# Kernel optimization log

Hardware: AMD Instinct MI355X
Metric: run time of the kernel (lower is better)

Reference implementation:

```python
import jax, jax.numpy as jnp
import numpy as np


def segment_softmax(x, seg, num_segments):
    # numerically-stable softmax over graph segments (rows of the sparse matrix)
    m = jax.ops.segment_max(x, seg, num_segments=num_segments)
    e = jnp.exp(x - m[seg])
    s = jax.ops.segment_sum(e, seg, num_segments=num_segments)
    return e / s[seg]


def setup_inputs() -> dict:
    key = jax.random.key(0)
    ks = jax.random.split(key, 12)
    B, N, E, P, H = 256, 51200, 102400, 5, 300
    instruction = jax.random.normal(ks[0], (B, H), dtype=jnp.float32)
    distribution = jax.random.uniform(ks[1], (N,), dtype=jnp.float32)
    node_attrs = jax.random.normal(ks[2], (N, H), dtype=jnp.float32)
    edge_attrs = jax.random.normal(ks[3], (E, H), dtype=jnp.float32)
    node_indices = jnp.sort(jax.random.randint(ks[4], (N,), 0, B)).astype(jnp.int32)
    edge_batch_indices = jax.random.randint(ks[5], (E,), 0, B).astype(jnp.int32)
    edge_indices = jax.random.randint(ks[6], (2, E), 0, N).astype(jnp.int32)
    prop_embeds = jax.random.normal(ks[7], (P, H), dtype=jnp.float32)
    Ws_property = jax.random.uniform(ks[8], (P, H, H), dtype=jnp.float32)
    W_state = jax.random.uniform(ks[9], (H,), dtype=jnp.float32)
    W_relation = jax.random.uniform(ks[10], (H,), dtype=jnp.float32)
    return {"instruction": instruction, "distribution": distribution, "node_attrs": node_attrs,
            "edge_attrs": edge_attrs, "node_indices": node_indices,
            "edge_batch_indices": edge_batch_indices, "edge_indices": edge_indices,
            "prop_embeds": prop_embeds, "Ws_property": Ws_property,
            "W_state": W_state, "W_relation": W_relation}


def reference(instruction, distribution, node_attrs, edge_attrs, node_indices,
              edge_batch_indices, edge_indices, prop_embeds, Ws_property,
              W_state, W_relation):
    B = instruction.shape[0]
    # [B, P] property similarities
    prop_sim = jax.nn.softmax(instruction @ prop_embeds.T, axis=1)
    ps_node = prop_sim[node_indices]            # [N, P]
    instr_node = instruction[node_indices]      # [N, H]
    # per-property transform of node attrs: [N, P-1, H]
    wx = jnp.einsum('phk,nk->nph', Ws_property[:-1], node_attrs)
    node_scores = jax.nn.elu(jnp.sum(ps_node[:, :-1, None] * instr_node[:, None, :] * wx, axis=1))  # [N, H]
    # relation transform of edge attrs: [E, H]
    edge_wx = jnp.einsum('hk,ek->eh', Ws_property[-1], edge_attrs)
    edge_scores = jax.nn.elu(instruction[edge_batch_indices] * edge_wx)  # [E, H]
    # per-graph (segment) softmax over state logits
    state_logits = node_scores @ W_state        # [N]
    next_states = segment_softmax(state_logits, node_indices, B)
    # scatter-add message passing: dst node accumulates distribution[src] * edge_scores
    agg = jnp.zeros_like(node_scores).at[edge_indices[1]].add(
        distribution[edge_indices[0], None] * edge_scores)  # [N, H]
    rel_logits = agg @ W_relation               # [N]
    next_relations = segment_softmax(rel_logits, node_indices, B)
    r = ps_node[:, -1]
    next_distribution = r * next_relations + (1.0 - r) * next_states
    return next_distribution, prop_sim
```

## Files before the change

kernel.cpp:

```cpp
#include <hip/hip_runtime.h>
#include <math.h>

#define H 300
#define PP 5
#define NE 128
#define KC 32
#define NCH 10
#define ROWB 128
#define WTILE (320 * ROWB)
#define WHALF (160 * ROWB)
#define ATILE (NE * ROWB)
#define NTHREADS 256
#define GT 512

using short8 = __attribute__((ext_vector_type(8))) short;
using f32x4  = __attribute__((ext_vector_type(4))) float;

__device__ __forceinline__ float wsum64(float v) {
#pragma unroll
    for (int m = 32; m >= 1; m >>= 1) v += __shfl_xor(v, m, 64);
    return v;
}
__device__ __forceinline__ float wmax64(float v) {
#pragma unroll
    for (int m = 32; m >= 1; m >>= 1) v = fmaxf(v, __shfl_xor(v, m, 64));
    return v;
}
__device__ __forceinline__ float eluf(float x) { return x > 0.f ? x : expm1f(x); }

__device__ __forceinline__ unsigned short f2bf(float x) {
    unsigned int u = __float_as_uint(x);
    unsigned int r = u + 0x7FFF + ((u >> 16) & 1);
    return (unsigned short)(r >> 16);
}
__device__ __forceinline__ float bf2f(unsigned short h) {
    return __uint_as_float(((unsigned int)h) << 16);
}
__device__ __forceinline__ int sw(int r, int kb) {
    return r * ROWB + (kb ^ ((r & 7) << 4));
}
__device__ __forceinline__ void split4(const float* v, uint2& ph, uint2& pl) {
    unsigned short hs[4], ls[4];
#pragma unroll
    for (int i = 0; i < 4; ++i) {
        hs[i] = f2bf(v[i]);
        ls[i] = f2bf(v[i] - bf2f(hs[i]));
    }
    ph = make_uint2((unsigned)hs[0] | ((unsigned)hs[1] << 16),
                    (unsigned)hs[2] | ((unsigned)hs[3] << 16));
    pl = make_uint2((unsigned)ls[0] | ((unsigned)ls[1] << 16),
                    (unsigned)ls[2] | ((unsigned)ls[3] << 16));
}
__device__ __forceinline__ void gload16(const void* g, void* lds) {
    __builtin_amdgcn_global_load_lds(
        (const __attribute__((address_space(1))) unsigned int*)g,
        (__attribute__((address_space(3))) unsigned int*)lds, 16, 0, 0);
}
#define SBAR() __builtin_amdgcn_s_barrier()
#define SCHED() __builtin_amdgcn_sched_barrier(0)
#define WAIT_LGKM() asm volatile("s_waitcnt lgkmcnt(0)" ::: "memory")
#define WAIT_VM0()  asm volatile("s_waitcnt vmcnt(0)" ::: "memory")
#define WAIT_VM4()  asm volatile("s_waitcnt vmcnt(4)" ::: "memory")
#define WAIT_VM5()  asm volatile("s_waitcnt vmcnt(5)" ::: "memory")

__global__ void k_prop_sim(const float* __restrict__ instr,
                           const float* __restrict__ pe,
                           float* __restrict__ prop_sim) {
    int b = blockIdx.x, lane = threadIdx.x;
    float dots[PP];
#pragma unroll
    for (int p = 0; p < PP; ++p) {
        float s = 0.f;
        for (int hh = lane; hh < H; hh += 64) s += instr[b * H + hh] * pe[p * H + hh];
        dots[p] = wsum64(s);
    }
    if (lane == 0) {
        float m = dots[0];
#pragma unroll
        for (int p = 1; p < PP; ++p) m = fmaxf(m, dots[p]);
        float e[PP], s = 0.f;
#pragma unroll
        for (int p = 0; p < PP; ++p) { e[p] = expf(dots[p] - m); s += e[p]; }
        float inv = 1.f / s;
#pragma unroll
        for (int p = 0; p < PP; ++p) prop_sim[b * PP + p] = e[p] * inv;
    }
}

__global__ void k_counts(const int* __restrict__ idx, int* __restrict__ counts, int N) {
    int i = blockIdx.x * blockDim.x + threadIdx.x;
    if (i < N) atomicAdd(&counts[idx[i]], 1);
}

__global__ void k_scan(const int* __restrict__ counts, int* __restrict__ offsets, int B) {
    __shared__ int sh[256];
    int t = threadIdx.x;
    int c = (t < B) ? counts[t] : 0;
    sh[t] = c;
    __syncthreads();
    for (int off = 1; off < 256; off <<= 1) {
        int v = (t >= off) ? sh[t - off] : 0;
        __syncthreads();
        sh[t] += v;
        __syncthreads();
    }
    if (t < B) offsets[t] = sh[t] - c;
    if (t == B - 1) offsets[B] = sh[t];
}

__global__ void k_presplit(const float* __restrict__ W4, char* __restrict__ img) {
    int c = blockIdx.x;
    int idx = blockIdx.y * NTHREADS + threadIdx.x;
    int r = idx >> 3, j = idx & 7;
    int k = c * KC + j * 4;
    float v[4] = {0.f, 0.f, 0.f, 0.f};
    if (r < H && k < H) *(float4*)v = *(const float4*)&W4[(size_t)r * H + k];
    uint2 ph, pl;
    split4(v, ph, pl);
    char* row = img + (size_t)c * WTILE + (size_t)r * ROWB;
    int x = (r & 7) << 4;
    *(uint2*)(row + ((j * 8) ^ x)) = ph;
    *(uint2*)(row + ((64 + j * 8) ^ x)) = pl;
}

__global__ void k_combine(const float* __restrict__ Ws,
                          const float* __restrict__ prop_sim,
                          const float* __restrict__ instr,
                          char* __restrict__ img) {
    int b = blockIdx.x, c = blockIdx.y, t = threadIdx.x;
    float ps0 = prop_sim[b * PP + 0], ps1 = prop_sim[b * PP + 1];
    float ps2 = prop_sim[b * PP + 2], ps3 = prop_sim[b * PP + 3];
    char* tile = img + ((size_t)b * NCH + c) * WTILE;
#pragma unroll
    for (int i = 0; i < 10; ++i) {
        int idx = t + i * NTHREADS;
        int r = idx >> 3, j = idx & 7;
        int k = c * KC + j * 4;
        float cv[4] = {0.f, 0.f, 0.f, 0.f};
        if (r < H && k < H) {
            float insv = instr[(size_t)b * H + r];
            size_t base = (size_t)r * H + k;
            float w0[4], w1[4], w2[4], w3[4];
            *(float4*)w0 = *(const float4*)&Ws[0 * (size_t)H * H + base];
            *(float4*)w1 = *(const float4*)&Ws[1 * (size_t)H * H + base];
            *(float4*)w2 = *(const float4*)&Ws[2 * (size_t)H * H + base];
            *(float4*)w3 = *(const float4*)&Ws[3 * (size_t)H * H + base];
#pragma unroll
            for (int q = 0; q < 4; ++q)
                cv[q] = insv * fmaf(ps0, w0[q], fmaf(ps1, w1[q], fmaf(ps2, w2[q], ps3 * w3[q])));
        }
        uint2 ph, pl;
        split4(cv, ph, pl);
        char* row = tile + (size_t)r * ROWB;
        int x = (r & 7) << 4;
        *(uint2*)(row + ((j * 8) ^ x)) = ph;
        *(uint2*)(row + ((64 + j * 8) ^ x)) = pl;
    }
}

__global__ __launch_bounds__(GT, 2) void k_gemm(
    const float* __restrict__ na, const float* __restrict__ ea,
    const char* __restrict__ Wc_img, const char* __restrict__ Wr_img,
    const float* __restrict__ instr, const float* __restrict__ wstate,
    const float* __restrict__ wrel,
    const int* __restrict__ offsets, const int* __restrict__ eb,
    const int* __restrict__ ei, const float* __restrict__ dist,
    float* __restrict__ slog, float* __restrict__ rlog,
    int N, int E, int nodeVX)
{
    __shared__ __align__(16) char W_t[2][WHALF];
    __shared__ __align__(16) char A_t[ATILE];

    int x = blockIdx.x;
    bool isNode = x < nodeVX;
    const float* Asrc;
    const char* Wsrc;
    int base, rowmax, b = 0, hz, nn = NE;
    if (isNode) {
        int gq = x / 48, r = x - gq * 48;
        int k = r >> 3;
        b = gq * 8 + (r & 7);
        int tile = k >> 1;
        hz = k & 1;
        int start = offsets[b], end = offsets[b + 1];
        base = start + tile * NE;
        if (base >= end) return;
        nn = min(NE, end - base);
        rowmax = N - 1;
        Asrc = na;
        Wsrc = Wc_img + (size_t)b * NCH * WTILE + (size_t)hz * WHALF;
    } else {
        int y = x - nodeVX;
        int gq = y / 16, r = y - gq * 16;
        int e = gq * 8 + (r & 7);
        hz = r >> 3;
        base = e * NE;
        rowmax = E - 1;
        Asrc = ea;
        Wsrc = Wr_img + (size_t)hz * WHALF;
    }

    int t = threadIdx.x;
    int w = t >> 6, l = t & 63, lane16 = l & 15, g = l >> 4;
    int wn = w & 3, wh = w >> 2;

    f32x4 acc[5][2];
#pragma unroll
    for (int ht = 0; ht < 5; ++ht)
#pragma unroll
        for (int cg = 0; cg < 2; ++cg) acc[ht][cg] = (f32x4){0.f, 0.f, 0.f, 0.f};

    float4 pa[2];

    auto loadA = [&](int c) {
#pragma unroll
        for (int i = 0; i < 2; ++i) {
            int idx = t + i * GT;
            int r = idx >> 3, j = idx & 7;
            int k = c * KC + j * 4;
            float4 v = {0.f, 0.f, 0.f, 0.f};
            if (k < H) {
                int row = min(base + r, rowmax);
                v = *(const float4*)&Asrc[(size_t)row * H + k];
            }
            pa[i] = v;
        }
    };
    auto storeA = [&]() {
#pragma unroll
        for (int i = 0; i < 2; ++i) {
            int idx = t + i * GT;
            int r = idx >> 3, j = idx & 7;
            float v[4] = {pa[i].x, pa[i].y, pa[i].z, pa[i].w};
            uint2 ph, pl;
            split4(v, ph, pl);
            *(uint2*)(A_t + sw(r, j * 8)) = ph;
            *(uint2*)(A_t + sw(r, 64 + j * 8)) = pl;
        }
    };
    auto gloadW = [&](int c, int sel) {
        const char* src = Wsrc + (size_t)c * WTILE;
        char* dst = W_t[sel];
        int off = w * 1024 + (l << 4);
        gload16(src + off, dst + off);
        gload16(src + 8192 + off, dst + 8192 + off);
        if (w < 4) gload16(src + 16384 + off, dst + 16384 + off);
    };

    loadA(0);
    gloadW(0, 0);
    storeA();
    loadA(1);
    gloadW(1, 1);
    SCHED();
    if (w < 4) { WAIT_VM5(); } else { WAIT_VM4(); }
    WAIT_LGKM();
    SBAR();
    SCHED();

    int curb = 0;
    for (int c = 0; c < NCH; ++c) {
        short8 bh[2], bl[2];
#pragma unroll
        for (int cg = 0; cg < 2; ++cg) {
            int brow = wn * 32 + cg * 16 + lane16;
            bh[cg] = *(const short8*)(A_t + sw(brow, g * 16));
            bl[cg] = *(const short8*)(A_t + sw(brow, 64 + g * 16));
        }
#pragma unroll
        for (int ht = 0; ht < 5; ++ht) {
            int arow = wh * 80 + ht * 16 + lane16;
            short8 ah = *(const short8*)(W_t[curb] + sw(arow, g * 16));
            short8 al = *(const short8*)(W_t[curb] + sw(arow, 64 + g * 16));
#pragma unroll
            for (int cg = 0; cg < 2; ++cg) {
                acc[ht][cg] = __builtin_amdgcn_mfma_f32_16x16x32_bf16(ah, bh[cg], acc[ht][cg], 0, 0, 0);
                acc[ht][cg] = __builtin_amdgcn_mfma_f32_16x16x32_bf16(ah, bl[cg], acc[ht][cg], 0, 0, 0);
                acc[ht][cg] = __builtin_amdgcn_mfma_f32_16x16x32_bf16(al, bh[cg], acc[ht][cg], 0, 0, 0);
            }
        }
        if (c + 1 < NCH) {
            WAIT_LGKM();
            SBAR();
            SCHED();
            storeA();
            if (c + 2 < NCH) {
                loadA(c + 2);
                gloadW(c + 2, curb);
                SCHED();
                if (w < 4) { WAIT_VM5(); } else { WAIT_VM4(); }
            } else {
                SCHED();
                WAIT_VM0();
            }
            WAIT_LGKM();
            SBAR();
            SCHED();
            curb ^= 1;
        }
    }

    if (isNode) {
#pragma unroll
        for (int cg = 0; cg < 2; ++cg) {
            float part = 0.f;
#pragma unroll
            for (int ht = 0; ht < 5; ++ht) {
                int hb = hz * 160 + wh * 80 + ht * 16 + g * 4;
#pragma unroll
                for (int r = 0; r < 4; ++r) {
                    int h = hb + r;
                    if (h < H) part += wstate[h] * eluf(acc[ht][cg][r]);
                }
            }
            part += __shfl_xor(part, 16, 64);
            part += __shfl_xor(part, 32, 64);
            int col = wn * 32 + cg * 16 + lane16;
            if (l < 16 && col < nn) atomicAdd(&slog[base + col], part);
        }
    } else {
#pragma unroll
        for (int cg = 0; cg < 2; ++cg) {
            int e = base + wn * 32 + cg * 16 + lane16;
            int be = eb[e];
            const float* insb = instr + (size_t)be * H;
            float part = 0.f;
#pragma unroll
            for (int ht = 0; ht < 5; ++ht) {
                int hb = hz * 160 + wh * 80 + ht * 16 + g * 4;
#pragma unroll
                for (int r = 0; r < 4; ++r) {
                    int h = hb + r;
                    if (h < H) part += wrel[h] * eluf(insb[h] * acc[ht][cg][r]);
                }
            }
            part += __shfl_xor(part, 16, 64);
            part += __shfl_xor(part, 32, 64);
            if (l < 16) atomicAdd(&rlog[ei[E + e]], dist[ei[e]] * part);
        }
    }
}

__global__ void k_final(const float* __restrict__ slog, const float* __restrict__ rlog,
                        const float* __restrict__ prop_sim, const int* __restrict__ offsets,
                        float* __restrict__ out)
{
    int b = blockIdx.x;
    int s0 = offsets[b], e1 = offsets[b + 1];
    int t = threadIdx.x, wave = t >> 6, lane = t & 63;
    __shared__ float shA[4], shB[4];
    float mS = -3.0e38f, mR = -3.0e38f;
    for (int i = s0 + t; i < e1; i += 256) {
        mS = fmaxf(mS, slog[i]);
        mR = fmaxf(mR, rlog[i]);
    }
    mS = wmax64(mS); mR = wmax64(mR);
    if (lane == 0) { shA[wave] = mS; shB[wave] = mR; }
    __syncthreads();
    mS = fmaxf(fmaxf(shA[0], shA[1]), fmaxf(shA[2], shA[3]));
    mR = fmaxf(fmaxf(shB[0], shB[1]), fmaxf(shB[2], shB[3]));
    __syncthreads();
    float sS = 0.f, sR = 0.f;
    for (int i = s0 + t; i < e1; i += 256) {
        sS += expf(slog[i] - mS);
        sR += expf(rlog[i] - mR);
    }
    sS = wsum64(sS); sR = wsum64(sR);
    if (lane == 0) { shA[wave] = sS; shB[wave] = sR; }
    __syncthreads();
    sS = shA[0] + shA[1] + shA[2] + shA[3];
    sR = shB[0] + shB[1] + shB[2] + shB[3];
    float r = prop_sim[b * PP + (PP - 1)];
    float iS = 1.f / sS, iR = 1.f / sR;
    for (int i = s0 + t; i < e1; i += 256) {
        float ns = expf(slog[i] - mS) * iS;
        float nr = expf(rlog[i] - mR) * iR;
        out[i] = r * nr + (1.f - r) * ns;
    }
}

extern "C" void kernel_launch(void* const* d_in, const int* in_sizes, int n_in,
                              void* d_out, int out_size, void* d_ws, size_t ws_size,
                              hipStream_t stream) {
    (void)n_in; (void)out_size; (void)ws_size;
    const float* instruction  = (const float*)d_in[0];
    const float* distribution = (const float*)d_in[1];
    const float* node_attrs   = (const float*)d_in[2];
    const float* edge_attrs   = (const float*)d_in[3];
    const int*   node_indices = (const int*)d_in[4];
    const int*   edge_batch   = (const int*)d_in[5];
    const int*   edge_indices = (const int*)d_in[6];
    const float* prop_embeds  = (const float*)d_in[7];
    const float* Ws           = (const float*)d_in[8];
    const float* W_state      = (const float*)d_in[9];
    const float* W_rel        = (const float*)d_in[10];

    int B = in_sizes[0] / H;
    int N = in_sizes[1];
    int E = in_sizes[5];

    float* out = (float*)d_out;
    float* prop_sim = out + N;

    float* ws = (float*)d_ws;
    float* state_logits = ws;
    float* rel_logits   = ws + N;
    int*   offsets      = (int*)(ws + 2 * (size_t)N);
    int*   counts       = offsets + (B + 1);
    uintptr_t wsp = (uintptr_t)(counts + B);
    wsp = (wsp + 255) & ~(uintptr_t)255;
    char* Wr_img = (char*)wsp;
    char* Wc_img = Wr_img + (size_t)NCH * WTILE;

    size_t zero_bytes = (size_t)2 * N * sizeof(float) + (size_t)(2 * B + 1) * sizeof(int);
    hipMemsetAsync(d_ws, 0, zero_bytes, stream);

    int nodeVX = 6 * B;
    int edgeVX = (E / NE) * 2;

    k_prop_sim<<<B, 64, 0, stream>>>(instruction, prop_embeds, prop_sim);
    k_presplit<<<dim3(NCH, 10), NTHREADS, 0, stream>>>(Ws + 4 * (size_t)H * H, Wr_img);
    k_counts<<<(N + 255) / 256, 256, 0, stream>>>(node_indices, counts, N);
    k_scan<<<1, 256, 0, stream>>>(counts, offsets, B);
    k_combine<<<dim3(B, NCH), NTHREADS, 0, stream>>>(Ws, prop_sim, instruction, Wc_img);
    k_gemm<<<nodeVX + edgeVX, GT, 0, stream>>>(
        node_attrs, edge_attrs, Wc_img, Wr_img, instruction, W_state, W_rel,
        offsets, edge_batch, edge_indices, distribution,
        state_logits, rel_logits, N, E, nodeVX);
    k_final<<<B, 256, 0, stream>>>(state_logits, rel_logits, prop_sim, offsets, out);
}
```

Measured before the change: 315.7 us.

## Double-buffer A tile in LDS and use packed bf16 convert for split

The activation tile in shared memory is now double-buffered, so the next chunk's bf16 hi/lo split and store can be issued right after the MFMA loop without first waiting on a barrier. The prefetch of chunk c+2 moves ahead of the barrier, and one LGKM wait is dropped, which shortens the synchronisation per chunk. The A-tile split also switches to the hardware v_cvt_pk_bf16_f32 instruction in place of manual bit-twiddled rounding. The cost is double the A tile LDS (another 16KB), which may reduce occupancy at 2 blocks per CU. The vmcnt wait counts may also no longer match the reordered loads.

```diff
diff --git a/kernel.cpp b/kernel.cpp
--- a/kernel.cpp
+++ b/kernel.cpp
@@ -39,7 +39,7 @@
 __device__ __forceinline__ int sw(int r, int kb) {
     return r * ROWB + (kb ^ ((r & 7) << 4));
 }
-__device__ __forceinline__ void split4(const float* v, uint2& ph, uint2& pl) {
+__device__ __forceinline__ void split4_bits(const float* v, uint2& ph, uint2& pl) {
     unsigned short hs[4], ls[4];
 #pragma unroll
     for (int i = 0; i < 4; ++i) {
@@ -50,6 +50,19 @@
                     (unsigned)hs[2] | ((unsigned)hs[3] << 16));
     pl = make_uint2((unsigned)ls[0] | ((unsigned)ls[1] << 16),
                     (unsigned)ls[2] | ((unsigned)ls[3] << 16));
+}
+__device__ __forceinline__ void split4_cvt(const float* v, uint2& ph, uint2& pl) {
+    unsigned h01, h23, l01, l23;
+    asm("v_cvt_pk_bf16_f32 %0, %1, %2" : "=v"(h01) : "v"(v[0]), "v"(v[1]));
+    asm("v_cvt_pk_bf16_f32 %0, %1, %2" : "=v"(h23) : "v"(v[2]), "v"(v[3]));
+    float r0 = v[0] - __uint_as_float(h01 << 16);
+    float r1 = v[1] - __uint_as_float(h01 & 0xffff0000u);
+    float r2 = v[2] - __uint_as_float(h23 << 16);
+    float r3 = v[3] - __uint_as_float(h23 & 0xffff0000u);
+    asm("v_cvt_pk_bf16_f32 %0, %1, %2" : "=v"(l01) : "v"(r0), "v"(r1));
+    asm("v_cvt_pk_bf16_f32 %0, %1, %2" : "=v"(l23) : "v"(r2), "v"(r3));
+    ph = make_uint2(h01, h23);
+    pl = make_uint2(l01, l23);
 }
 __device__ __forceinline__ void gload16(const void* g, void* lds) {
     __builtin_amdgcn_global_load_lds(
@@ -116,7 +129,7 @@
     float v[4] = {0.f, 0.f, 0.f, 0.f};
     if (r < H && k < H) *(float4*)v = *(const float4*)&W4[(size_t)r * H + k];
     uint2 ph, pl;
-    split4(v, ph, pl);
+    split4_bits(v, ph, pl);
     char* row = img + (size_t)c * WTILE + (size_t)r * ROWB;
     int x = (r & 7) << 4;
     *(uint2*)(row + ((j * 8) ^ x)) = ph;
@@ -150,7 +163,7 @@
                 cv[q] = insv * fmaf(ps0, w0[q], fmaf(ps1, w1[q], fmaf(ps2, w2[q], ps3 * w3[q])));
         }
         uint2 ph, pl;
-        split4(cv, ph, pl);
+        split4_bits(cv, ph, pl);
         char* row = tile + (size_t)r * ROWB;
         int x = (r & 7) << 4;
         *(uint2*)(row + ((j * 8) ^ x)) = ph;
@@ -169,7 +182,7 @@
     int N, int E, int nodeVX)
 {
     __shared__ __align__(16) char W_t[2][WHALF];
-    __shared__ __align__(16) char A_t[ATILE];
+    __shared__ __align__(16) char A_t[2][ATILE];
 
     int x = blockIdx.x;
     bool isNode = x < nodeVX;
@@ -226,16 +239,16 @@
             pa[i] = v;
         }
     };
-    auto storeA = [&]() {
+    auto storeA = [&](int sel) {
 #pragma unroll
         for (int i = 0; i < 2; ++i) {
             int idx = t + i * GT;
             int r = idx >> 3, j = idx & 7;
             float v[4] = {pa[i].x, pa[i].y, pa[i].z, pa[i].w};
             uint2 ph, pl;
-            split4(v, ph, pl);
-            *(uint2*)(A_t + sw(r, j * 8)) = ph;
-            *(uint2*)(A_t + sw(r, 64 + j * 8)) = pl;
+            split4_cvt(v, ph, pl);
+            *(uint2*)(A_t[sel] + sw(r, j * 8)) = ph;
+            *(uint2*)(A_t[sel] + sw(r, 64 + j * 8)) = pl;
         }
     };
     auto gloadW = [&](int c, int sel) {
@@ -249,7 +262,7 @@
 
     loadA(0);
     gloadW(0, 0);
-    storeA();
+    storeA(0);
     loadA(1);
     gloadW(1, 1);
     SCHED();
@@ -258,20 +271,20 @@
     SBAR();
     SCHED();
 
-    int curb = 0;
     for (int c = 0; c < NCH; ++c) {
+        int cur = c & 1;
         short8 bh[2], bl[2];
 #pragma unroll
         for (int cg = 0; cg < 2; ++cg) {
             int brow = wn * 32 + cg * 16 + lane16;
-            bh[cg] = *(const short8*)(A_t + sw(brow, g * 16));
-            bl[cg] = *(const short8*)(A_t + sw(brow, 64 + g * 16));
+            bh[cg] = *(const short8*)(A_t[cur] + sw(brow, g * 16));
+            bl[cg] = *(const short8*)(A_t[cur] + sw(brow, 64 + g * 16));
         }
 #pragma unroll
         for (int ht = 0; ht < 5; ++ht) {
             int arow = wh * 80 + ht * 16 + lane16;
-            short8 ah = *(const short8*)(W_t[curb] + sw(arow, g * 16));
-            short8 al = *(const short8*)(W_t[curb] + sw(arow, 64 + g * 16));
+            short8 ah = *(const short8*)(W_t[cur] + sw(arow, g * 16));
+            short8 al = *(const short8*)(W_t[cur] + sw(arow, 64 + g * 16));
 #pragma unroll
             for (int cg = 0; cg < 2; ++cg) {
                 acc[ht][cg] = __builtin_amdgcn_mfma_f32_16x16x32_bf16(ah, bh[cg], acc[ht][cg], 0, 0, 0);
@@ -280,23 +293,20 @@
             }
         }
         if (c + 1 < NCH) {
+            storeA(cur ^ 1);
+            if (c + 2 < NCH) loadA(c + 2);
             WAIT_LGKM();
             SBAR();
             SCHED();
-            storeA();
             if (c + 2 < NCH) {
-                loadA(c + 2);
-                gloadW(c + 2, curb);
+                gloadW(c + 2, cur);
                 SCHED();
                 if (w < 4) { WAIT_VM5(); } else { WAIT_VM4(); }
             } else {
-                SCHED();
                 WAIT_VM0();
             }
-            WAIT_LGKM();
             SBAR();
             SCHED();
-            curb ^= 1;
         }
     }
 
```

Result: faster. 298.2 us, median of 2 (-5.5%).
